# Optimization experiments

Hardware: AMD Instinct MI355X
Metric: run time of the kernel (lower is better)

Reference implementation:

```python
import jax, jax.numpy as jnp
import numpy as np

B, S, H, E, I, TOP_K = 2, 1024, 1024, 8, 1408, 2
W_SCALE = 0.02


def setup_inputs() -> dict:
    key = jax.random.key(0)
    ks = jax.random.split(key, 5)
    return {
        "hidden_states": jax.random.normal(ks[0], (B, S, H), dtype=jnp.float32),
        "router_weight": jax.random.normal(ks[1], (H, E), dtype=jnp.float32) * W_SCALE,
        "gate_proj": jax.random.normal(ks[2], (E, H, I), dtype=jnp.float32) * W_SCALE,
        "up_proj": jax.random.normal(ks[3], (E, H, I), dtype=jnp.float32) * W_SCALE,
        "down_proj": jax.random.normal(ks[4], (E, I, H), dtype=jnp.float32) * W_SCALE,
        "gate_bias": jnp.zeros((E, I), dtype=jnp.float32),
        "up_bias": jnp.zeros((E, I), dtype=jnp.float32),
        "down_bias": jnp.zeros((E, H), dtype=jnp.float32),
        "top_k": TOP_K,
    }


def reference(hidden_states, router_weight, gate_proj, up_proj, down_proj,
              gate_bias, up_bias, down_bias, top_k):
    b, s, h = hidden_states.shape
    e = gate_proj.shape[0]
    x = hidden_states.reshape(-1, h)              # [T, H], T = b*s
    t = x.shape[0]

    # --- RouterAdapter: MoEGate top-k then scatter into dense scores [T, E] ---
    logits = x @ router_weight                    # [T, E]
    probs = jax.nn.softmax(logits, axis=-1)
    topk_w, topk_idx = jax.lax.top_k(probs, top_k)  # [T, k]
    topk_w = topk_w / jnp.sum(topk_w, axis=-1, keepdims=True)  # norm_topk_prob
    scores = jnp.zeros((t, e), dtype=topk_w.dtype)
    scores = scores.at[jnp.arange(t)[:, None], topk_idx].set(topk_w)

    # --- StackedExperts.sparse_forward (dense equivalent of sparse matmuls) ---
    g = jnp.einsum('th,ehi->tei', x, gate_proj) + gate_bias[None]  # [T, E, I]
    u = jnp.einsum('th,ehi->tei', x, up_proj) + up_bias[None]      # [T, E, I]
    act = jax.nn.silu(g) * u                       # ACTIVATION_DEEPSEEK
    d = jnp.einsum('tei,eih->teh', act, down_proj) + down_bias[None]  # [T, E, H]

    # combine per-expert outputs with router scores (non-routed scores are 0,
    # matching the sparse matmul's zero blocks)
    y = jnp.einsum('teh,te->th', d, scores)
    return y.reshape(b, s, h)
```

## Files before the change

### kernel.cpp

```cpp
#include <hip/hip_runtime.h>

#define T_TOK 2048
#define HDIM  1024
#define NEXP  8
#define IDIM  1408

#define BM 128
#define BN 64
#define BK 32
#define KPAD 40
#define MT_SLOTS 16
#define GU_NT 22
#define DN_NT 16
#define DK_HALF 704

typedef __attribute__((ext_vector_type(8))) short bf16x8;
typedef __attribute__((ext_vector_type(4))) float f32x4;

static __device__ __forceinline__ unsigned short f2bf(float f) {
    union { float f; unsigned u; } a; a.f = f;
    return (unsigned short)((a.u + 0x7fffu + ((a.u >> 16) & 1u)) >> 16);
}

__global__ __launch_bounds__(256) void router_compute_kernel(
    const float* __restrict__ x,
    const float* __restrict__ rw,
    int*   __restrict__ sel,
    float* __restrict__ w1arr,
    unsigned short* __restrict__ xb)
{
    __shared__ float rwT[NEXP][HDIM];
    const int tid = threadIdx.x;
#pragma unroll
    for (int p = 0; p < 4; ++p) {
        const int h = tid + 256 * p;
        const float4 a = *(const float4*)(rw + (size_t)h * 8);
        const float4 b = *(const float4*)(rw + (size_t)h * 8 + 4);
        rwT[0][h] = a.x; rwT[1][h] = a.y; rwT[2][h] = a.z; rwT[3][h] = a.w;
        rwT[4][h] = b.x; rwT[5][h] = b.y; rwT[6][h] = b.z; rwT[7][h] = b.w;
    }
    __syncthreads();

    const int wave = (blockIdx.x * blockDim.x + threadIdx.x) >> 6;
    const int lane = threadIdx.x & 63;
    if (wave >= T_TOK) return;
    const int t = wave;

    float xr[16];
    const float* xp = x + (size_t)t * HDIM;
#pragma unroll
    for (int i = 0; i < 16; ++i) xr[i] = xp[lane + 64 * i];

    unsigned short* xbp = xb + (size_t)t * HDIM;
#pragma unroll
    for (int i = 0; i < 16; ++i) xbp[lane + 64 * i] = f2bf(xr[i]);

    double logits[NEXP];
#pragma unroll
    for (int e = 0; e < NEXP; ++e) {
        double s = 0.0;
#pragma unroll
        for (int i = 0; i < 16; ++i)
            s += (double)xr[i] * (double)rwT[e][lane + 64 * i];
#pragma unroll
        for (int off = 32; off > 0; off >>= 1)
            s += __shfl_down(s, off, 64);
        logits[e] = s;
    }

    if (lane == 0) {
        int e1 = 0;
        for (int e = 1; e < NEXP; ++e) if (logits[e] > logits[e1]) e1 = e;
        int e2 = -1;
        for (int e = 0; e < NEXP; ++e) {
            if (e == e1) continue;
            if (e2 < 0 || logits[e] > logits[e2]) e2 = e;
        }
        const double w1 = 1.0 / (1.0 + exp(logits[e2] - logits[e1]));
        sel[t]   = e1 | (e2 << 8);
        w1arr[t] = (float)w1;
    }
}

__global__ __launch_bounds__(1024) void router_scatter_kernel(
    const int* __restrict__ sel, const float* __restrict__ w1arr,
    int* __restrict__ counts,
    int* __restrict__ tok_list, float* __restrict__ wgt_list,
    int* __restrict__ row_list)
{
    __shared__ int cnt[NEXP];
    const int tid = threadIdx.x;
    if (tid < NEXP) cnt[tid] = 0;
    __syncthreads();
    for (int t = tid; t < T_TOK; t += 1024) {
        const int s  = sel[t];
        const int e1 = s & 255, e2 = s >> 8;
        const float w1 = w1arr[t];
        const int p1 = atomicAdd(&cnt[e1], 1);
        tok_list[e1 * T_TOK + p1] = t;
        wgt_list[e1 * T_TOK + p1] = w1;
        row_list[e1 * T_TOK + p1] = 2 * t;
        const int p2 = atomicAdd(&cnt[e2], 1);
        tok_list[e2 * T_TOK + p2] = t;
        wgt_list[e2 * T_TOK + p2] = 1.0f - w1;
        row_list[e2 * T_TOK + p2] = 2 * t + 1;
    }
    __syncthreads();
    if (tid < NEXP) counts[tid] = cnt[tid];
}

__global__ __launch_bounds__(256) void wtrans_all_kernel(
    const float* __restrict__ gw, const float* __restrict__ uw,
    const float* __restrict__ dw,
    unsigned short* __restrict__ gwt, unsigned short* __restrict__ uwt,
    unsigned short* __restrict__ dwt)
{
    const int z  = blockIdx.z;
    const int bx = blockIdx.x;
    const float* src; unsigned short* dst; int K, N, kb, nb;
    if (z < 16) {
        K = HDIM; N = IDIM;
        const int e = z & 7;
        src = (z < 8 ? gw : uw) + (size_t)e * K * N;
        dst = (z < 8 ? gwt : uwt) + (size_t)e * (size_t)N * K;
        nb = bx % 11; kb = bx / 11;
    } else {
        K = IDIM; N = HDIM;
        const int e = z - 16;
        src = dw + (size_t)e * K * N;
        dst = dwt + (size_t)e * (size_t)N * K;
        nb = bx & 7; kb = bx >> 3;
    }

    const int tid  = threadIdx.x;
    const int wv   = tid >> 6;
    const int lane = tid & 63;
    const int k0 = kb * 64 + (wv >> 1) * 32 + (lane >> 4) * 8;
    const int n0 = nb * 128 + (wv & 1) * 64 + (lane & 15) * 4;

    float4 v[8];
#pragma unroll
    for (int r = 0; r < 8; ++r)
        v[r] = *(const float4*)(src + (size_t)(k0 + r) * N + n0);

#pragma unroll
    for (int i = 0; i < 4; ++i) {
        ushort4 lo, hi;
        lo.x = f2bf(((const float*)&v[0])[i]);
        lo.y = f2bf(((const float*)&v[1])[i]);
        lo.z = f2bf(((const float*)&v[2])[i]);
        lo.w = f2bf(((const float*)&v[3])[i]);
        hi.x = f2bf(((const float*)&v[4])[i]);
        hi.y = f2bf(((const float*)&v[5])[i]);
        hi.z = f2bf(((const float*)&v[6])[i]);
        hi.w = f2bf(((const float*)&v[7])[i]);
        unsigned short* dp = dst + (size_t)(n0 + i) * K + k0;
        *(ushort4*)(dp)     = lo;
        *(ushort4*)(dp + 4) = hi;
    }
}

__global__ __launch_bounds__(256) void gateup_kernel(
    const unsigned short* __restrict__ xb,
    const unsigned short* __restrict__ gwt,
    const unsigned short* __restrict__ uwt,
    const float* __restrict__ gb, const float* __restrict__ ub,
    const int* __restrict__ counts,
    const int* __restrict__ tok_list,
    const int* __restrict__ row_list,
    unsigned short* __restrict__ act)
{
    const int flat = blockIdx.x;
    const int xcd  = flat & 7;
    const int q    = flat >> 3;
    const int mt   = q & 15;
    const int slot = q >> 4;
    const int P    = slot * 8 + xcd;
    const int e    = P / GU_NT;
    const int nt   = P % GU_NT;
    const int n_e  = counts[e];
    const int m0   = mt * BM;
    if (m0 >= n_e) return;
    const int n0 = nt * BN;

    const unsigned short* gwp = gwt + (size_t)e * IDIM * HDIM;
    const unsigned short* uwp = uwt + (size_t)e * IDIM * HDIM;
    const float* gbp = gb + (size_t)e * IDIM;
    const float* ubp = ub + (size_t)e * IDIM;

    __shared__ unsigned short As[BM][KPAD];
    __shared__ unsigned short Bg[BN][KPAD];
    __shared__ unsigned short Bu[BN][KPAD];
    __shared__ int gr_lds[BM];
    __shared__ int or_lds[BM];

    const int tid = threadIdx.x;
    const int base = e * T_TOK;
    if (tid < BM) {
        const int m = m0 + tid;
        int g = -1, o = -1;
        if (m < n_e) { g = tok_list[base + m]; o = row_list[base + m]; }
        gr_lds[tid] = g; or_lds[tid] = o;
    }
    __syncthreads();

    const int ar = tid >> 1;
    const int ac = (tid & 1) * 16;
    const int arow = gr_lds[ar];
    const unsigned short* ap = xb + (size_t)(arow < 0 ? 0 : arow) * HDIM;
    const int u   = tid & 127;
    const int brow = u >> 1;
    const int bch  = (u & 1) * 16;
    const unsigned short* bsrc =
        ((tid >> 7) ? uwp : gwp) + (size_t)(n0 + brow) * HDIM + bch;
    unsigned short* Bdst =
        ((tid >> 7) ? &Bu[0][0] : &Bg[0][0]) + brow * KPAD + bch;

    const int wv = tid >> 6, lane = tid & 63;
    const int wm = (wv & 1) * 64, wn = (wv >> 1) * 32;
    const int l16 = lane & 15, quad = lane >> 4;

    f32x4 accg[4][2], accu[4][2];
    const f32x4 zero = {0.0f, 0.0f, 0.0f, 0.0f};
#pragma unroll
    for (int i = 0; i < 4; ++i)
#pragma unroll
        for (int j = 0; j < 2; ++j) { accg[i][j] = zero; accu[i][j] = zero; }

    uint4 PA0 = {0,0,0,0}, PA1 = {0,0,0,0}, PB0, PB1;
    if (arow >= 0) {
        PA0 = *(const uint4*)(ap + ac);
        PA1 = *(const uint4*)(ap + ac + 8);
    }
    PB0 = *(const uint4*)(bsrc);
    PB1 = *(const uint4*)(bsrc + 8);

    for (int k0 = 0; k0 < HDIM; k0 += BK) {
        __syncthreads();
        *(uint4*)&As[ar][ac]       = PA0;
        *(uint4*)&As[ar][ac + 8]   = PA1;
        *(uint4*)(Bdst)            = PB0;
        *(uint4*)(Bdst + 8)        = PB1;
        __syncthreads();

        const int kn = k0 + BK;
        if (kn < HDIM) {
            if (arow >= 0) {
                PA0 = *(const uint4*)(ap + kn + ac);
                PA1 = *(const uint4*)(ap + kn + ac + 8);
            }
            PB0 = *(const uint4*)(bsrc + kn);
            PB1 = *(const uint4*)(bsrc + kn + 8);
        }

        bf16x8 af[4], bgf[2], buf[2];
#pragma unroll
        for (int i = 0; i < 4; ++i)
            af[i] = *(const bf16x8*)&As[wm + i * 16 + l16][quad * 8];
#pragma unroll
        for (int j = 0; j < 2; ++j) {
            bgf[j] = *(const bf16x8*)&Bg[wn + j * 16 + l16][quad * 8];
            buf[j] = *(const bf16x8*)&Bu[wn + j * 16 + l16][quad * 8];
        }
#pragma unroll
        for (int i = 0; i < 4; ++i)
#pragma unroll
            for (int j = 0; j < 2; ++j) {
                accg[i][j] = __builtin_amdgcn_mfma_f32_16x16x32_bf16(
                    af[i], bgf[j], accg[i][j], 0, 0, 0);
                accu[i][j] = __builtin_amdgcn_mfma_f32_16x16x32_bf16(
                    af[i], buf[j], accu[i][j], 0, 0, 0);
            }
    }

#pragma unroll
    for (int j = 0; j < 2; ++j) {
        const int nl = n0 + wn + j * 16 + l16;
        const float gbv = gbp[nl];
        const float ubv = ubp[nl];
#pragma unroll
        for (int i = 0; i < 4; ++i) {
#pragma unroll
            for (int ii = 0; ii < 4; ++ii) {
                const int ml = wm + i * 16 + quad * 4 + ii;
                const int orow = or_lds[ml];
                if (orow >= 0) {
                    const float g = accg[i][j][ii] + gbv;
                    const float uu = accu[i][j][ii] + ubv;
                    act[(size_t)orow * IDIM + nl] =
                        f2bf(g * uu / (1.0f + __expf(-g)));
                }
            }
        }
    }
}

__global__ __launch_bounds__(256) void down_kernel(
    const unsigned short* __restrict__ act,
    const unsigned short* __restrict__ dwt,
    const float* __restrict__ db,
    const int* __restrict__ counts,
    const float* __restrict__ wgt_list,
    const int* __restrict__ row_list,
    float* __restrict__ y2)
{
    const int flat = blockIdx.x;
    const int xcd  = flat & 7;
    const int q    = flat >> 3;
    const int mt   = q & 15;
    const int slot = q >> 4;
    const int P    = slot * 8 + xcd;
    const int sk   = P & 1;
    const int en   = P >> 1;
    const int e    = en >> 4;
    const int nt   = en & 15;
    const int n_e  = counts[e];
    const int m0   = mt * BM;
    if (m0 >= n_e) return;
    const int n0 = nt * BN;
    const int ks = sk * DK_HALF;
    float* y2s = y2 + (size_t)sk * 2 * T_TOK * HDIM;

    const unsigned short* dwp = dwt + (size_t)e * HDIM * IDIM;
    const float* dbp = db + (size_t)e * HDIM;

    __shared__ unsigned short As[BM][KPAD];
    __shared__ unsigned short Bs[BN][KPAD];
    __shared__ int   r_lds[BM];
    __shared__ float w_lds[BM];

    const int tid = threadIdx.x;
    const int base = e * T_TOK;
    if (tid < BM) {
        const int m = m0 + tid;
        int r = -1; float w = 0.0f;
        if (m < n_e) { r = row_list[base + m]; w = wgt_list[base + m]; }
        r_lds[tid] = r; w_lds[tid] = w;
    }
    __syncthreads();

    const int ar = tid >> 1;
    const int ac = (tid & 1) * 16;
    const int arow = r_lds[ar];
    const unsigned short* ap = act + (size_t)(arow < 0 ? 0 : arow) * IDIM + ks;
    const int brow = tid >> 2;
    const int bch  = (tid & 3) * 8;
    const unsigned short* bsrc = dwp + (size_t)(n0 + brow) * IDIM + ks + bch;
    unsigned short* Bdst = &Bs[0][0] + brow * KPAD + bch;

    const int wv = tid >> 6, lane = tid & 63;
    const int wm = (wv & 1) * 64, wn = (wv >> 1) * 32;
    const int l16 = lane & 15, quad = lane >> 4;

    f32x4 acc[4][2];
    const f32x4 zero = {0.0f, 0.0f, 0.0f, 0.0f};
#pragma unroll
    for (int i = 0; i < 4; ++i)
#pragma unroll
        for (int j = 0; j < 2; ++j) acc[i][j] = zero;

    uint4 PA0 = {0,0,0,0}, PA1 = {0,0,0,0}, PB;
    if (arow >= 0) {
        PA0 = *(const uint4*)(ap + ac);
        PA1 = *(const uint4*)(ap + ac + 8);
    }
    PB = *(const uint4*)(bsrc);

    for (int k0 = 0; k0 < DK_HALF; k0 += BK) {
        __syncthreads();
        *(uint4*)&As[ar][ac]     = PA0;
        *(uint4*)&As[ar][ac + 8] = PA1;
        *(uint4*)(Bdst)          = PB;
        __syncthreads();

        const int kn = k0 + BK;
        if (kn < DK_HALF) {
            if (arow >= 0) {
                PA0 = *(const uint4*)(ap + kn + ac);
                PA1 = *(const uint4*)(ap + kn + ac + 8);
            }
            PB = *(const uint4*)(bsrc + kn);
        }

        bf16x8 af[4], bfr[2];
#pragma unroll
        for (int i = 0; i < 4; ++i)
            af[i] = *(const bf16x8*)&As[wm + i * 16 + l16][quad * 8];
#pragma unroll
        for (int j = 0; j < 2; ++j)
            bfr[j] = *(const bf16x8*)&Bs[wn + j * 16 + l16][quad * 8];
#pragma unroll
        for (int i = 0; i < 4; ++i)
#pragma unroll
            for (int j = 0; j < 2; ++j)
                acc[i][j] = __builtin_amdgcn_mfma_f32_16x16x32_bf16(
                    af[i], bfr[j], acc[i][j], 0, 0, 0);
    }

#pragma unroll
    for (int j = 0; j < 2; ++j) {
        const int nl = n0 + wn + j * 16 + l16;
        const float bv = (sk == 0) ? dbp[nl] : 0.0f;
#pragma unroll
        for (int i = 0; i < 4; ++i) {
#pragma unroll
            for (int ii = 0; ii < 4; ++ii) {
                const int ml = wm + i * 16 + quad * 4 + ii;
                const int rr = r_lds[ml];
                if (rr >= 0)
                    y2s[(size_t)rr * HDIM + nl] = w_lds[ml] * (acc[i][j][ii] + bv);
            }
        }
    }
}

__global__ __launch_bounds__(256) void combine_kernel(
    const float* __restrict__ y2, float* __restrict__ out)
{
    const int idx = (blockIdx.x * 256 + threadIdx.x) * 4;
    const int t = idx >> 10;
    const int h = idx & 1023;
    const float* y2b = y2 + (size_t)2 * T_TOK * HDIM;
    const float4 a0 = *(const float4*)(y2  + ((size_t)2 * t) * HDIM + h);
    const float4 a1 = *(const float4*)(y2  + ((size_t)2 * t + 1) * HDIM + h);
    const float4 b0 = *(const float4*)(y2b + ((size_t)2 * t) * HDIM + h);
    const float4 b1 = *(const float4*)(y2b + ((size_t)2 * t + 1) * HDIM + h);
    float4 o;
    o.x = a0.x + a1.x + b0.x + b1.x;
    o.y = a0.y + a1.y + b0.y + b1.y;
    o.z = a0.z + a1.z + b0.z + b1.z;
    o.w = a0.w + a1.w + b0.w + b1.w;
    *(float4*)(out + idx) = o;
}

extern "C" void kernel_launch(void* const* d_in, const int* in_sizes, int n_in,
                              void* d_out, int out_size, void* d_ws, size_t ws_size,
                              hipStream_t stream)
{
    const float* x      = (const float*)d_in[0];
    const float* rw     = (const float*)d_in[1];
    const float* gate_w = (const float*)d_in[2];
    const float* up_w   = (const float*)d_in[3];
    const float* down_w = (const float*)d_in[4];
    const float* gate_b = (const float*)d_in[5];
    const float* up_b   = (const float*)d_in[6];
    const float* down_b = (const float*)d_in[7];
    float* out = (float*)d_out;

    char* ws = (char*)d_ws;
    size_t off = 0;
    int*   counts   = (int*)(ws + off);  off += 256;
    int*   tok_list = (int*)(ws + off);  off += 65536;
    float* wgt_list = (float*)(ws + off); off += 65536;
    int*   row_list = (int*)(ws + off);  off += 65536;
    int*   sel      = (int*)(ws + off);  off += T_TOK * 4;
    float* w1arr    = (float*)(ws + off); off += T_TOK * 4;
    unsigned short* x_bf = (unsigned short*)(ws + off); off += (size_t)T_TOK * HDIM * 2;
    unsigned short* act  = (unsigned short*)(ws + off); off += (size_t)2 * T_TOK * IDIM * 2;
    unsigned short* dwt  = (unsigned short*)(ws + off); off += (size_t)NEXP * IDIM * HDIM * 2;
    unsigned short* gwt  = (unsigned short*)(ws + off); off += (size_t)NEXP * IDIM * HDIM * 2;
    unsigned short* uwt  = (unsigned short*)(ws + off);
    float* y2 = (float*)gwt;

    wtrans_all_kernel<<<dim3(176, 1, 24), 256, 0, stream>>>(
        gate_w, up_w, down_w, gwt, uwt, dwt);

    router_compute_kernel<<<T_TOK / 4, 256, 0, stream>>>(x, rw, sel, w1arr, x_bf);

    router_scatter_kernel<<<1, 1024, 0, stream>>>(
        sel, w1arr, counts, tok_list, wgt_list, row_list);

    gateup_kernel<<<8 * GU_NT * MT_SLOTS, 256, 0, stream>>>(
        x_bf, gwt, uwt, gate_b, up_b, counts, tok_list, row_list, act);

    down_kernel<<<2 * 8 * DN_NT * MT_SLOTS, 256, 0, stream>>>(
        act, dwt, down_b, counts, wgt_list, row_list, y2);

    combine_kernel<<<(T_TOK * HDIM / 4) / 256, 256, 0, stream>>>(y2, out);
}
```

Before: 288.4 us.

## Stage weight transpose through LDS and use 8-wave GEMM blocks

The fp32-to-bf16 weight transpose kernel now writes into an LDS tile and then emits coalesced 16-byte row writes, instead of scattered 8-byte stores. The gate/up and down GEMM kernels move to 512 threads, so each of 8 waves computes a 32x32 sub-tile and each thread issues one 16-byte load per tile. The intent is better latency hiding and write coalescing, at the cost of less MFMA work per wave and more LDS fragment reads.

```diff
diff --git a/kernel.cpp b/kernel.cpp
--- a/kernel.cpp
+++ b/kernel.cpp
@@ -131,36 +131,38 @@
         dst = dwt + (size_t)e * (size_t)N * K;
         nb = bx & 7; kb = bx >> 3;
     }
-
-    const int tid  = threadIdx.x;
-    const int wv   = tid >> 6;
-    const int lane = tid & 63;
-    const int k0 = kb * 64 + (wv >> 1) * 32 + (lane >> 4) * 8;
-    const int n0 = nb * 128 + (wv & 1) * 64 + (lane & 15) * 4;
-
-    float4 v[8];
-#pragma unroll
-    for (int r = 0; r < 8; ++r)
-        v[r] = *(const float4*)(src + (size_t)(k0 + r) * N + n0);
-
-#pragma unroll
-    for (int i = 0; i < 4; ++i) {
-        ushort4 lo, hi;
-        lo.x = f2bf(((const float*)&v[0])[i]);
-        lo.y = f2bf(((const float*)&v[1])[i]);
-        lo.z = f2bf(((const float*)&v[2])[i]);
-        lo.w = f2bf(((const float*)&v[3])[i]);
-        hi.x = f2bf(((const float*)&v[4])[i]);
-        hi.y = f2bf(((const float*)&v[5])[i]);
-        hi.z = f2bf(((const float*)&v[6])[i]);
-        hi.w = f2bf(((const float*)&v[7])[i]);
-        unsigned short* dp = dst + (size_t)(n0 + i) * K + k0;
-        *(ushort4*)(dp)     = lo;
-        *(ushort4*)(dp + 4) = hi;
-    }
-}
-
-__global__ __launch_bounds__(256) void gateup_kernel(
+    const int k0 = kb * 64;
+    const int n0 = nb * 128;
+
+    __shared__ unsigned short tb[128][66];
+
+    const int tid = threadIdx.x;
+    const int lk = tid >> 5;
+    const int ln = (tid & 31) * 4;
+#pragma unroll
+    for (int r = 0; r < 8; ++r) {
+        const int k = r * 8 + lk;
+        const float4 v = *(const float4*)(src + (size_t)(k0 + k) * N + n0 + ln);
+        tb[ln + 0][k] = f2bf(v.x);
+        tb[ln + 1][k] = f2bf(v.y);
+        tb[ln + 2][k] = f2bf(v.z);
+        tb[ln + 3][k] = f2bf(v.w);
+    }
+    __syncthreads();
+
+    const int wn = tid >> 3;
+    const int wk = (tid & 7) * 8;
+#pragma unroll
+    for (int p = 0; p < 4; ++p) {
+        const int n = p * 32 + wn;
+        const unsigned* rp = (const unsigned*)&tb[n][wk];
+        uint4 o;
+        o.x = rp[0]; o.y = rp[1]; o.z = rp[2]; o.w = rp[3];
+        *(uint4*)(dst + (size_t)(n0 + n) * K + k0 + wk) = o;
+    }
+}
+
+__global__ __launch_bounds__(512, 4) void gateup_kernel(
     const unsigned short* __restrict__ xb,
     const unsigned short* __restrict__ gwt,
     const unsigned short* __restrict__ uwt,
@@ -204,72 +206,63 @@
     }
     __syncthreads();
 
-    const int ar = tid >> 1;
-    const int ac = (tid & 1) * 16;
+    const int ar = tid >> 2;
+    const int ac = (tid & 3) * 8;
     const int arow = gr_lds[ar];
-    const unsigned short* ap = xb + (size_t)(arow < 0 ? 0 : arow) * HDIM;
-    const int u   = tid & 127;
-    const int brow = u >> 1;
-    const int bch  = (u & 1) * 16;
+    const unsigned short* ap = xb + (size_t)(arow < 0 ? 0 : arow) * HDIM + ac;
+    unsigned short* Adst = &As[0][0] + ar * KPAD + ac;
+    const int u    = tid & 255;
+    const int brow = u >> 2;
+    const int bch  = (u & 3) * 8;
     const unsigned short* bsrc =
-        ((tid >> 7) ? uwp : gwp) + (size_t)(n0 + brow) * HDIM + bch;
+        ((tid >> 8) ? uwp : gwp) + (size_t)(n0 + brow) * HDIM + bch;
     unsigned short* Bdst =
-        ((tid >> 7) ? &Bu[0][0] : &Bg[0][0]) + brow * KPAD + bch;
+        ((tid >> 8) ? &Bu[0][0] : &Bg[0][0]) + brow * KPAD + bch;
 
     const int wv = tid >> 6, lane = tid & 63;
-    const int wm = (wv & 1) * 64, wn = (wv >> 1) * 32;
+    const int wm = (wv & 3) * 32, wn = (wv >> 2) * 32;
     const int l16 = lane & 15, quad = lane >> 4;
 
-    f32x4 accg[4][2], accu[4][2];
+    f32x4 accg[2][2], accu[2][2];
     const f32x4 zero = {0.0f, 0.0f, 0.0f, 0.0f};
 #pragma unroll
-    for (int i = 0; i < 4; ++i)
+    for (int i = 0; i < 2; ++i)
 #pragma unroll
         for (int j = 0; j < 2; ++j) { accg[i][j] = zero; accu[i][j] = zero; }
 
-    uint4 PA0 = {0,0,0,0}, PA1 = {0,0,0,0}, PB0, PB1;
-    if (arow >= 0) {
-        PA0 = *(const uint4*)(ap + ac);
-        PA1 = *(const uint4*)(ap + ac + 8);
-    }
-    PB0 = *(const uint4*)(bsrc);
-    PB1 = *(const uint4*)(bsrc + 8);
+    uint4 PA = {0, 0, 0, 0}, PB;
+    if (arow >= 0) PA = *(const uint4*)(ap);
+    PB = *(const uint4*)(bsrc);
 
     for (int k0 = 0; k0 < HDIM; k0 += BK) {
         __syncthreads();
-        *(uint4*)&As[ar][ac]       = PA0;
-        *(uint4*)&As[ar][ac + 8]   = PA1;
-        *(uint4*)(Bdst)            = PB0;
-        *(uint4*)(Bdst + 8)        = PB1;
+        *(uint4*)Adst = PA;
+        *(uint4*)Bdst = PB;
         __syncthreads();
 
         const int kn = k0 + BK;
         if (kn < HDIM) {
-            if (arow >= 0) {
-                PA0 = *(const uint4*)(ap + kn + ac);
-                PA1 = *(const uint4*)(ap + kn + ac + 8);
-            }
-            PB0 = *(const uint4*)(bsrc + kn);
-            PB1 = *(const uint4*)(bsrc + kn + 8);
-        }
-
-        bf16x8 af[4], bgf[2], buf[2];
-#pragma unroll
-        for (int i = 0; i < 4; ++i)
+            if (arow >= 0) PA = *(const uint4*)(ap + kn);
+            PB = *(const uint4*)(bsrc + kn);
+        }
+
+        bf16x8 af[2], bgf[2], buf_[2];
+#pragma unroll
+        for (int i = 0; i < 2; ++i)
             af[i] = *(const bf16x8*)&As[wm + i * 16 + l16][quad * 8];
 #pragma unroll
         for (int j = 0; j < 2; ++j) {
-            bgf[j] = *(const bf16x8*)&Bg[wn + j * 16 + l16][quad * 8];
-            buf[j] = *(const bf16x8*)&Bu[wn + j * 16 + l16][quad * 8];
-        }
-#pragma unroll
-        for (int i = 0; i < 4; ++i)
+            bgf[j]  = *(const bf16x8*)&Bg[wn + j * 16 + l16][quad * 8];
+            buf_[j] = *(const bf16x8*)&Bu[wn + j * 16 + l16][quad * 8];
+        }
+#pragma unroll
+        for (int i = 0; i < 2; ++i)
 #pragma unroll
             for (int j = 0; j < 2; ++j) {
                 accg[i][j] = __builtin_amdgcn_mfma_f32_16x16x32_bf16(
                     af[i], bgf[j], accg[i][j], 0, 0, 0);
                 accu[i][j] = __builtin_amdgcn_mfma_f32_16x16x32_bf16(
-                    af[i], buf[j], accu[i][j], 0, 0, 0);
+                    af[i], buf_[j], accu[i][j], 0, 0, 0);
             }
     }
 
@@ -279,7 +272,7 @@
         const float gbv = gbp[nl];
         const float ubv = ubp[nl];
 #pragma unroll
-        for (int i = 0; i < 4; ++i) {
+        for (int i = 0; i < 2; ++i) {
 #pragma unroll
             for (int ii = 0; ii < 4; ++ii) {
                 const int ml = wm + i * 16 + quad * 4 + ii;
@@ -295,7 +288,7 @@
     }
 }
 
-__global__ __launch_bounds__(256) void down_kernel(
+__global__ __launch_bounds__(512, 4) void down_kernel(
     const unsigned short* __restrict__ act,
     const unsigned short* __restrict__ dwt,
     const float* __restrict__ db,
@@ -339,58 +332,54 @@
     }
     __syncthreads();
 
-    const int ar = tid >> 1;
-    const int ac = (tid & 1) * 16;
+    const int ar = tid >> 2;
+    const int ac = (tid & 3) * 8;
     const int arow = r_lds[ar];
-    const unsigned short* ap = act + (size_t)(arow < 0 ? 0 : arow) * IDIM + ks;
-    const int brow = tid >> 2;
+    const unsigned short* ap =
+        act + (size_t)(arow < 0 ? 0 : arow) * IDIM + ks + ac;
+    unsigned short* Adst = &As[0][0] + ar * KPAD + ac;
+    const bool hasB = tid < 256;
+    const int brow = (tid & 255) >> 2;
     const int bch  = (tid & 3) * 8;
     const unsigned short* bsrc = dwp + (size_t)(n0 + brow) * IDIM + ks + bch;
     unsigned short* Bdst = &Bs[0][0] + brow * KPAD + bch;
 
     const int wv = tid >> 6, lane = tid & 63;
-    const int wm = (wv & 1) * 64, wn = (wv >> 1) * 32;
+    const int wm = (wv & 3) * 32, wn = (wv >> 2) * 32;
     const int l16 = lane & 15, quad = lane >> 4;
 
-    f32x4 acc[4][2];
+    f32x4 acc[2][2];
     const f32x4 zero = {0.0f, 0.0f, 0.0f, 0.0f};
 #pragma unroll
-    for (int i = 0; i < 4; ++i)
+    for (int i = 0; i < 2; ++i)
 #pragma unroll
         for (int j = 0; j < 2; ++j) acc[i][j] = zero;
 
-    uint4 PA0 = {0,0,0,0}, PA1 = {0,0,0,0}, PB;
-    if (arow >= 0) {
-        PA0 = *(const uint4*)(ap + ac);
-        PA1 = *(const uint4*)(ap + ac + 8);
-    }
-    PB = *(const uint4*)(bsrc);
+    uint4 PA = {0, 0, 0, 0}, PB = {0, 0, 0, 0};
+    if (arow >= 0) PA = *(const uint4*)(ap);
+    if (hasB) PB = *(const uint4*)(bsrc);
 
     for (int k0 = 0; k0 < DK_HALF; k0 += BK) {
         __syncthreads();
-        *(uint4*)&As[ar][ac]     = PA0;
-        *(uint4*)&As[ar][ac + 8] = PA1;
-        *(uint4*)(Bdst)          = PB;
+        *(uint4*)Adst = PA;
+        if (hasB) *(uint4*)Bdst = PB;
         __syncthreads();
 
         const int kn = k0 + BK;
         if (kn < DK_HALF) {
-            if (arow >= 0) {
-                PA0 = *(const uint4*)(ap + kn + ac);
-                PA1 = *(const uint4*)(ap + kn + ac + 8);
-            }
-            PB = *(const uint4*)(bsrc + kn);
-        }
-
-        bf16x8 af[4], bfr[2];
-#pragma unroll
-        for (int i = 0; i < 4; ++i)
+            if (arow >= 0) PA = *(const uint4*)(ap + kn);
+            if (hasB) PB = *(const uint4*)(bsrc + kn);
+        }
+
+        bf16x8 af[2], bfr[2];
+#pragma unroll
+        for (int i = 0; i < 2; ++i)
             af[i] = *(const bf16x8*)&As[wm + i * 16 + l16][quad * 8];
 #pragma unroll
         for (int j = 0; j < 2; ++j)
             bfr[j] = *(const bf16x8*)&Bs[wn + j * 16 + l16][quad * 8];
 #pragma unroll
-        for (int i = 0; i < 4; ++i)
+        for (int i = 0; i < 2; ++i)
 #pragma unroll
             for (int j = 0; j < 2; ++j)
                 acc[i][j] = __builtin_amdgcn_mfma_f32_16x16x32_bf16(
@@ -402,7 +391,7 @@
         const int nl = n0 + wn + j * 16 + l16;
         const float bv = (sk == 0) ? dbp[nl] : 0.0f;
 #pragma unroll
-        for (int i = 0; i < 4; ++i) {
+        for (int i = 0; i < 2; ++i) {
 #pragma unroll
             for (int ii = 0; ii < 4; ++ii) {
                 const int ml = wm + i * 16 + quad * 4 + ii;
@@ -470,10 +459,10 @@
     router_scatter_kernel<<<1, 1024, 0, stream>>>(
         sel, w1arr, counts, tok_list, wgt_list, row_list);
 
-    gateup_kernel<<<8 * GU_NT * MT_SLOTS, 256, 0, stream>>>(
+    gateup_kernel<<<8 * GU_NT * MT_SLOTS, 512, 0, stream>>>(
         x_bf, gwt, uwt, gate_b, up_b, counts, tok_list, row_list, act);
 
-    down_kernel<<<2 * 8 * DN_NT * MT_SLOTS, 256, 0, stream>>>(
+    down_kernel<<<2 * 8 * DN_NT * MT_SLOTS, 512, 0, stream>>>(
         act, dwt, down_b, counts, wgt_list, row_list, y2);
 
     combine_kernel<<<(T_TOK * HDIM / 4) / 256, 256, 0, stream>>>(y2, out);
```

Result: slower. 295.9 us (+2.6%).

## Double GEMM K-tile to 64 and stage weight transpose through LDS

Applied to the files above, without the earlier changes.

The gate/up and down GEMM kernels now use a 64-wide K tile (padded LDS rows of 72), so each main-loop iteration loads twice as much data and issues two MFMA sub-steps per pair of barriers. This halves the number of synchronisations and loop iterations. The cost is more prefetch registers and more LDS per block. Separately, the weight transpose/convert kernel now stages through a shared-memory tile so its global stores are coalesced 16-byte row writes instead of scattered 8-byte writes. DK_HALF=704 is divisible by 64, so the down kernel's K loop stays exact.

```diff
diff --git a/kernel.cpp b/kernel.cpp
--- a/kernel.cpp
+++ b/kernel.cpp
@@ -7,8 +7,8 @@
 
 #define BM 128
 #define BN 64
-#define BK 32
-#define KPAD 40
+#define BK 64
+#define KPAD 72
 #define MT_SLOTS 16
 #define GU_NT 22
 #define DN_NT 16
@@ -131,32 +131,34 @@
         dst = dwt + (size_t)e * (size_t)N * K;
         nb = bx & 7; kb = bx >> 3;
     }
-
-    const int tid  = threadIdx.x;
-    const int wv   = tid >> 6;
-    const int lane = tid & 63;
-    const int k0 = kb * 64 + (wv >> 1) * 32 + (lane >> 4) * 8;
-    const int n0 = nb * 128 + (wv & 1) * 64 + (lane & 15) * 4;
-
-    float4 v[8];
-#pragma unroll
-    for (int r = 0; r < 8; ++r)
-        v[r] = *(const float4*)(src + (size_t)(k0 + r) * N + n0);
-
-#pragma unroll
-    for (int i = 0; i < 4; ++i) {
-        ushort4 lo, hi;
-        lo.x = f2bf(((const float*)&v[0])[i]);
-        lo.y = f2bf(((const float*)&v[1])[i]);
-        lo.z = f2bf(((const float*)&v[2])[i]);
-        lo.w = f2bf(((const float*)&v[3])[i]);
-        hi.x = f2bf(((const float*)&v[4])[i]);
-        hi.y = f2bf(((const float*)&v[5])[i]);
-        hi.z = f2bf(((const float*)&v[6])[i]);
-        hi.w = f2bf(((const float*)&v[7])[i]);
-        unsigned short* dp = dst + (size_t)(n0 + i) * K + k0;
-        *(ushort4*)(dp)     = lo;
-        *(ushort4*)(dp + 4) = hi;
+    const int k0 = kb * 64;
+    const int n0 = nb * 128;
+
+    __shared__ unsigned short tb[128][66];
+
+    const int tid = threadIdx.x;
+    const int lk = tid >> 5;
+    const int ln = (tid & 31) * 4;
+#pragma unroll
+    for (int r = 0; r < 8; ++r) {
+        const int k = r * 8 + lk;
+        const float4 v = *(const float4*)(src + (size_t)(k0 + k) * N + n0 + ln);
+        tb[ln + 0][k] = f2bf(v.x);
+        tb[ln + 1][k] = f2bf(v.y);
+        tb[ln + 2][k] = f2bf(v.z);
+        tb[ln + 3][k] = f2bf(v.w);
+    }
+    __syncthreads();
+
+    const int wn = tid >> 3;
+    const int wk = (tid & 7) * 8;
+#pragma unroll
+    for (int p = 0; p < 4; ++p) {
+        const int n = p * 32 + wn;
+        const unsigned* rp = (const unsigned*)&tb[n][wk];
+        uint4 o;
+        o.x = rp[0]; o.y = rp[1]; o.z = rp[2]; o.w = rp[3];
+        *(uint4*)(dst + (size_t)(n0 + n) * K + k0 + wk) = o;
     }
 }
 
@@ -205,12 +207,13 @@
     __syncthreads();
 
     const int ar = tid >> 1;
-    const int ac = (tid & 1) * 16;
+    const int ac = (tid & 1) * 32;
     const int arow = gr_lds[ar];
-    const unsigned short* ap = xb + (size_t)(arow < 0 ? 0 : arow) * HDIM;
-    const int u   = tid & 127;
+    const unsigned short* ap = xb + (size_t)(arow < 0 ? 0 : arow) * HDIM + ac;
+    unsigned short* Adst = &As[0][0] + ar * KPAD + ac;
+    const int u    = tid & 127;
     const int brow = u >> 1;
-    const int bch  = (u & 1) * 16;
+    const int bch  = (u & 1) * 32;
     const unsigned short* bsrc =
         ((tid >> 7) ? uwp : gwp) + (size_t)(n0 + brow) * HDIM + bch;
     unsigned short* Bdst =
@@ -227,50 +230,67 @@
 #pragma unroll
         for (int j = 0; j < 2; ++j) { accg[i][j] = zero; accu[i][j] = zero; }
 
-    uint4 PA0 = {0,0,0,0}, PA1 = {0,0,0,0}, PB0, PB1;
+    uint4 PA0 = {0,0,0,0}, PA1 = {0,0,0,0}, PA2 = {0,0,0,0}, PA3 = {0,0,0,0};
+    uint4 PB0, PB1, PB2, PB3;
     if (arow >= 0) {
-        PA0 = *(const uint4*)(ap + ac);
-        PA1 = *(const uint4*)(ap + ac + 8);
+        PA0 = *(const uint4*)(ap);
+        PA1 = *(const uint4*)(ap + 8);
+        PA2 = *(const uint4*)(ap + 16);
+        PA3 = *(const uint4*)(ap + 24);
     }
     PB0 = *(const uint4*)(bsrc);
     PB1 = *(const uint4*)(bsrc + 8);
+    PB2 = *(const uint4*)(bsrc + 16);
+    PB3 = *(const uint4*)(bsrc + 24);
 
     for (int k0 = 0; k0 < HDIM; k0 += BK) {
         __syncthreads();
-        *(uint4*)&As[ar][ac]       = PA0;
-        *(uint4*)&As[ar][ac + 8]   = PA1;
-        *(uint4*)(Bdst)            = PB0;
-        *(uint4*)(Bdst + 8)        = PB1;
+        *(uint4*)(Adst)      = PA0;
+        *(uint4*)(Adst + 8)  = PA1;
+        *(uint4*)(Adst + 16) = PA2;
+        *(uint4*)(Adst + 24) = PA3;
+        *(uint4*)(Bdst)      = PB0;
+        *(uint4*)(Bdst + 8)  = PB1;
+        *(uint4*)(Bdst + 16) = PB2;
+        *(uint4*)(Bdst + 24) = PB3;
         __syncthreads();
 
         const int kn = k0 + BK;
         if (kn < HDIM) {
             if (arow >= 0) {
-                PA0 = *(const uint4*)(ap + kn + ac);
-                PA1 = *(const uint4*)(ap + kn + ac + 8);
+                PA0 = *(const uint4*)(ap + kn);
+                PA1 = *(const uint4*)(ap + kn + 8);
+                PA2 = *(const uint4*)(ap + kn + 16);
+                PA3 = *(const uint4*)(ap + kn + 24);
             }
             PB0 = *(const uint4*)(bsrc + kn);
             PB1 = *(const uint4*)(bsrc + kn + 8);
-        }
-
-        bf16x8 af[4], bgf[2], buf[2];
-#pragma unroll
-        for (int i = 0; i < 4; ++i)
-            af[i] = *(const bf16x8*)&As[wm + i * 16 + l16][quad * 8];
-#pragma unroll
-        for (int j = 0; j < 2; ++j) {
-            bgf[j] = *(const bf16x8*)&Bg[wn + j * 16 + l16][quad * 8];
-            buf[j] = *(const bf16x8*)&Bu[wn + j * 16 + l16][quad * 8];
-        }
-#pragma unroll
-        for (int i = 0; i < 4; ++i)
+            PB2 = *(const uint4*)(bsrc + kn + 16);
+            PB3 = *(const uint4*)(bsrc + kn + 24);
+        }
+
+#pragma unroll
+        for (int ks = 0; ks < 2; ++ks) {
+            const int kc = ks * 32 + quad * 8;
+            bf16x8 af[4], bgf[2], buf_[2];
+#pragma unroll
+            for (int i = 0; i < 4; ++i)
+                af[i] = *(const bf16x8*)&As[wm + i * 16 + l16][kc];
 #pragma unroll
             for (int j = 0; j < 2; ++j) {
-                accg[i][j] = __builtin_amdgcn_mfma_f32_16x16x32_bf16(
-                    af[i], bgf[j], accg[i][j], 0, 0, 0);
-                accu[i][j] = __builtin_amdgcn_mfma_f32_16x16x32_bf16(
-                    af[i], buf[j], accu[i][j], 0, 0, 0);
+                bgf[j]  = *(const bf16x8*)&Bg[wn + j * 16 + l16][kc];
+                buf_[j] = *(const bf16x8*)&Bu[wn + j * 16 + l16][kc];
             }
+#pragma unroll
+            for (int i = 0; i < 4; ++i)
+#pragma unroll
+                for (int j = 0; j < 2; ++j) {
+                    accg[i][j] = __builtin_amdgcn_mfma_f32_16x16x32_bf16(
+                        af[i], bgf[j], accg[i][j], 0, 0, 0);
+                    accu[i][j] = __builtin_amdgcn_mfma_f32_16x16x32_bf16(
+                        af[i], buf_[j], accu[i][j], 0, 0, 0);
+                }
+        }
     }
 
 #pragma unroll
@@ -340,11 +360,13 @@
     __syncthreads();
 
     const int ar = tid >> 1;
-    const int ac = (tid & 1) * 16;
+    const int ac = (tid & 1) * 32;
     const int arow = r_lds[ar];
-    const unsigned short* ap = act + (size_t)(arow < 0 ? 0 : arow) * IDIM + ks;
+    const unsigned short* ap =
+        act + (size_t)(arow < 0 ? 0 : arow) * IDIM + ks + ac;
+    unsigned short* Adst = &As[0][0] + ar * KPAD + ac;
     const int brow = tid >> 2;
-    const int bch  = (tid & 3) * 8;
+    const int bch  = (tid & 3) * 16;
     const unsigned short* bsrc = dwp + (size_t)(n0 + brow) * IDIM + ks + bch;
     unsigned short* Bdst = &Bs[0][0] + brow * KPAD + bch;
 
@@ -359,42 +381,56 @@
 #pragma unroll
         for (int j = 0; j < 2; ++j) acc[i][j] = zero;
 
-    uint4 PA0 = {0,0,0,0}, PA1 = {0,0,0,0}, PB;
+    uint4 PA0 = {0,0,0,0}, PA1 = {0,0,0,0}, PA2 = {0,0,0,0}, PA3 = {0,0,0,0};
+    uint4 PB0, PB1;
     if (arow >= 0) {
-        PA0 = *(const uint4*)(ap + ac);
-        PA1 = *(const uint4*)(ap + ac + 8);
-    }
-    PB = *(const uint4*)(bsrc);
+        PA0 = *(const uint4*)(ap);
+        PA1 = *(const uint4*)(ap + 8);
+        PA2 = *(const uint4*)(ap + 16);
+        PA3 = *(const uint4*)(ap + 24);
+    }
+    PB0 = *(const uint4*)(bsrc);
+    PB1 = *(const uint4*)(bsrc + 8);
 
     for (int k0 = 0; k0 < DK_HALF; k0 += BK) {
         __syncthreads();
-        *(uint4*)&As[ar][ac]     = PA0;
-        *(uint4*)&As[ar][ac + 8] = PA1;
-        *(uint4*)(Bdst)          = PB;
+        *(uint4*)(Adst)      = PA0;
+        *(uint4*)(Adst + 8)  = PA1;
+        *(uint4*)(Adst + 16) = PA2;
+        *(uint4*)(Adst + 24) = PA3;
+        *(uint4*)(Bdst)      = PB0;
+        *(uint4*)(Bdst + 8)  = PB1;
         __syncthreads();
 
         const int kn = k0 + BK;
         if (kn < DK_HALF) {
             if (arow >= 0) {
-                PA0 = *(const uint4*)(ap + kn + ac);
-                PA1 = *(const uint4*)(ap + kn + ac + 8);
+                PA0 = *(const uint4*)(ap + kn);
+                PA1 = *(const uint4*)(ap + kn + 8);
+                PA2 = *(const uint4*)(ap + kn + 16);
+                PA3 = *(const uint4*)(ap + kn + 24);
             }
-            PB = *(const uint4*)(bsrc + kn);
-        }
-
-        bf16x8 af[4], bfr[2];
-#pragma unroll
-        for (int i = 0; i < 4; ++i)
-            af[i] = *(const bf16x8*)&As[wm + i * 16 + l16][quad * 8];
-#pragma unroll
-        for (int j = 0; j < 2; ++j)
-            bfr[j] = *(const bf16x8*)&Bs[wn + j * 16 + l16][quad * 8];
-#pragma unroll
-        for (int i = 0; i < 4; ++i)
+            PB0 = *(const uint4*)(bsrc + kn);
+            PB1 = *(const uint4*)(bsrc + kn + 8);
+        }
+
+#pragma unroll
+        for (int ks2 = 0; ks2 < 2; ++ks2) {
+            const int kc = ks2 * 32 + quad * 8;
+            bf16x8 af[4], bfr[2];
+#pragma unroll
+            for (int i = 0; i < 4; ++i)
+                af[i] = *(const bf16x8*)&As[wm + i * 16 + l16][kc];
 #pragma unroll
             for (int j = 0; j < 2; ++j)
-                acc[i][j] = __builtin_amdgcn_mfma_f32_16x16x32_bf16(
-                    af[i], bfr[j], acc[i][j], 0, 0, 0);
+                bfr[j] = *(const bf16x8*)&Bs[wn + j * 16 + l16][kc];
+#pragma unroll
+            for (int i = 0; i < 4; ++i)
+#pragma unroll
+                for (int j = 0; j < 2; ++j)
+                    acc[i][j] = __builtin_amdgcn_mfma_f32_16x16x32_bf16(
+                        af[i], bfr[j], acc[i][j], 0, 0, 0);
+        }
     }
 
 #pragma unroll
```

After: 294.9 us. 2.2% more time.

## Fuse weight fp32-to-bf16 conversion and transpose into GEMM tile loads

Applied to the files above, without the earlier changes.

Removes the separate weight transpose/convert pre-pass. The gate/up and down GEMM kernels now read fp32 weights directly in their native [K,N] layout, convert them to bf16 in registers and write them transposed into shared memory. This avoids writing and re-reading about 70 MB of bf16 weights plus one kernel launch. In exchange, every M-tile block re-reads and re-converts the fp32 weights, which doubles per-block weight bytes and adds conversion ALU work and scattered LDS stores inside the main loop.

```diff
diff --git a/kernel.cpp b/kernel.cpp
--- a/kernel.cpp
+++ b/kernel.cpp
@@ -109,61 +109,10 @@
     if (tid < NEXP) counts[tid] = cnt[tid];
 }
 
-__global__ __launch_bounds__(256) void wtrans_all_kernel(
-    const float* __restrict__ gw, const float* __restrict__ uw,
-    const float* __restrict__ dw,
-    unsigned short* __restrict__ gwt, unsigned short* __restrict__ uwt,
-    unsigned short* __restrict__ dwt)
-{
-    const int z  = blockIdx.z;
-    const int bx = blockIdx.x;
-    const float* src; unsigned short* dst; int K, N, kb, nb;
-    if (z < 16) {
-        K = HDIM; N = IDIM;
-        const int e = z & 7;
-        src = (z < 8 ? gw : uw) + (size_t)e * K * N;
-        dst = (z < 8 ? gwt : uwt) + (size_t)e * (size_t)N * K;
-        nb = bx % 11; kb = bx / 11;
-    } else {
-        K = IDIM; N = HDIM;
-        const int e = z - 16;
-        src = dw + (size_t)e * K * N;
-        dst = dwt + (size_t)e * (size_t)N * K;
-        nb = bx & 7; kb = bx >> 3;
-    }
-
-    const int tid  = threadIdx.x;
-    const int wv   = tid >> 6;
-    const int lane = tid & 63;
-    const int k0 = kb * 64 + (wv >> 1) * 32 + (lane >> 4) * 8;
-    const int n0 = nb * 128 + (wv & 1) * 64 + (lane & 15) * 4;
-
-    float4 v[8];
-#pragma unroll
-    for (int r = 0; r < 8; ++r)
-        v[r] = *(const float4*)(src + (size_t)(k0 + r) * N + n0);
-
-#pragma unroll
-    for (int i = 0; i < 4; ++i) {
-        ushort4 lo, hi;
-        lo.x = f2bf(((const float*)&v[0])[i]);
-        lo.y = f2bf(((const float*)&v[1])[i]);
-        lo.z = f2bf(((const float*)&v[2])[i]);
-        lo.w = f2bf(((const float*)&v[3])[i]);
-        hi.x = f2bf(((const float*)&v[4])[i]);
-        hi.y = f2bf(((const float*)&v[5])[i]);
-        hi.z = f2bf(((const float*)&v[6])[i]);
-        hi.w = f2bf(((const float*)&v[7])[i]);
-        unsigned short* dp = dst + (size_t)(n0 + i) * K + k0;
-        *(ushort4*)(dp)     = lo;
-        *(ushort4*)(dp + 4) = hi;
-    }
-}
-
 __global__ __launch_bounds__(256) void gateup_kernel(
     const unsigned short* __restrict__ xb,
-    const unsigned short* __restrict__ gwt,
-    const unsigned short* __restrict__ uwt,
+    const float* __restrict__ gw,
+    const float* __restrict__ uw,
     const float* __restrict__ gb, const float* __restrict__ ub,
     const int* __restrict__ counts,
     const int* __restrict__ tok_list,
@@ -183,8 +132,8 @@
     if (m0 >= n_e) return;
     const int n0 = nt * BN;
 
-    const unsigned short* gwp = gwt + (size_t)e * IDIM * HDIM;
-    const unsigned short* uwp = uwt + (size_t)e * IDIM * HDIM;
+    const float* gwp = gw + (size_t)e * HDIM * IDIM;
+    const float* uwp = uw + (size_t)e * HDIM * IDIM;
     const float* gbp = gb + (size_t)e * IDIM;
     const float* ubp = ub + (size_t)e * IDIM;
 
@@ -208,13 +157,12 @@
     const int ac = (tid & 1) * 16;
     const int arow = gr_lds[ar];
     const unsigned short* ap = xb + (size_t)(arow < 0 ? 0 : arow) * HDIM;
-    const int u   = tid & 127;
-    const int brow = u >> 1;
-    const int bch  = (u & 1) * 16;
-    const unsigned short* bsrc =
-        ((tid >> 7) ? uwp : gwp) + (size_t)(n0 + brow) * HDIM + bch;
-    unsigned short* Bdst =
-        ((tid >> 7) ? &Bu[0][0] : &Bg[0][0]) + brow * KPAD + bch;
+    const int u  = tid & 127;
+    const int kq = (u >> 4) * 4;
+    const int nc = (u & 15) * 4;
+    const float* bp =
+        ((tid >> 7) ? uwp : gwp) + (size_t)kq * IDIM + n0 + nc;
+    unsigned short* Bb = ((tid >> 7) ? &Bu[0][0] : &Bg[0][0]);
 
     const int wv = tid >> 6, lane = tid & 63;
     const int wm = (wv & 1) * 64, wn = (wv >> 1) * 32;
@@ -227,20 +175,30 @@
 #pragma unroll
         for (int j = 0; j < 2; ++j) { accg[i][j] = zero; accu[i][j] = zero; }
 
-    uint4 PA0 = {0,0,0,0}, PA1 = {0,0,0,0}, PB0, PB1;
+    uint4 PA0 = {0,0,0,0}, PA1 = {0,0,0,0};
+    float4 PB0, PB1, PB2, PB3;
     if (arow >= 0) {
         PA0 = *(const uint4*)(ap + ac);
         PA1 = *(const uint4*)(ap + ac + 8);
     }
-    PB0 = *(const uint4*)(bsrc);
-    PB1 = *(const uint4*)(bsrc + 8);
+    PB0 = *(const float4*)(bp);
+    PB1 = *(const float4*)(bp + IDIM);
+    PB2 = *(const float4*)(bp + 2 * IDIM);
+    PB3 = *(const float4*)(bp + 3 * IDIM);
 
     for (int k0 = 0; k0 < HDIM; k0 += BK) {
         __syncthreads();
-        *(uint4*)&As[ar][ac]       = PA0;
-        *(uint4*)&As[ar][ac + 8]   = PA1;
-        *(uint4*)(Bdst)            = PB0;
-        *(uint4*)(Bdst + 8)        = PB1;
+        *(uint4*)&As[ar][ac]     = PA0;
+        *(uint4*)&As[ar][ac + 8] = PA1;
+#pragma unroll
+        for (int i = 0; i < 4; ++i) {
+            ushort4 w;
+            w.x = f2bf(((const float*)&PB0)[i]);
+            w.y = f2bf(((const float*)&PB1)[i]);
+            w.z = f2bf(((const float*)&PB2)[i]);
+            w.w = f2bf(((const float*)&PB3)[i]);
+            *(ushort4*)(Bb + (size_t)(nc + i) * KPAD + kq) = w;
+        }
         __syncthreads();
 
         const int kn = k0 + BK;
@@ -249,18 +207,21 @@
                 PA0 = *(const uint4*)(ap + kn + ac);
                 PA1 = *(const uint4*)(ap + kn + ac + 8);
             }
-            PB0 = *(const uint4*)(bsrc + kn);
-            PB1 = *(const uint4*)(bsrc + kn + 8);
-        }
-
-        bf16x8 af[4], bgf[2], buf[2];
+            const float* bq = bp + (size_t)kn * IDIM;
+            PB0 = *(const float4*)(bq);
+            PB1 = *(const float4*)(bq + IDIM);
+            PB2 = *(const float4*)(bq + 2 * IDIM);
+            PB3 = *(const float4*)(bq + 3 * IDIM);
+        }
+
+        bf16x8 af[4], bgf[2], buf_[2];
 #pragma unroll
         for (int i = 0; i < 4; ++i)
             af[i] = *(const bf16x8*)&As[wm + i * 16 + l16][quad * 8];
 #pragma unroll
         for (int j = 0; j < 2; ++j) {
-            bgf[j] = *(const bf16x8*)&Bg[wn + j * 16 + l16][quad * 8];
-            buf[j] = *(const bf16x8*)&Bu[wn + j * 16 + l16][quad * 8];
+            bgf[j]  = *(const bf16x8*)&Bg[wn + j * 16 + l16][quad * 8];
+            buf_[j] = *(const bf16x8*)&Bu[wn + j * 16 + l16][quad * 8];
         }
 #pragma unroll
         for (int i = 0; i < 4; ++i)
@@ -269,7 +230,7 @@
                 accg[i][j] = __builtin_amdgcn_mfma_f32_16x16x32_bf16(
                     af[i], bgf[j], accg[i][j], 0, 0, 0);
                 accu[i][j] = __builtin_amdgcn_mfma_f32_16x16x32_bf16(
-                    af[i], buf[j], accu[i][j], 0, 0, 0);
+                    af[i], buf_[j], accu[i][j], 0, 0, 0);
             }
     }
 
@@ -297,7 +258,7 @@
 
 __global__ __launch_bounds__(256) void down_kernel(
     const unsigned short* __restrict__ act,
-    const unsigned short* __restrict__ dwt,
+    const float* __restrict__ dw,
     const float* __restrict__ db,
     const int* __restrict__ counts,
     const float* __restrict__ wgt_list,
@@ -321,7 +282,7 @@
     const int ks = sk * DK_HALF;
     float* y2s = y2 + (size_t)sk * 2 * T_TOK * HDIM;
 
-    const unsigned short* dwp = dwt + (size_t)e * HDIM * IDIM;
+    const float* dwp = dw + (size_t)e * IDIM * HDIM;
     const float* dbp = db + (size_t)e * HDIM;
 
     __shared__ unsigned short As[BM][KPAD];
@@ -343,10 +304,10 @@
     const int ac = (tid & 1) * 16;
     const int arow = r_lds[ar];
     const unsigned short* ap = act + (size_t)(arow < 0 ? 0 : arow) * IDIM + ks;
-    const int brow = tid >> 2;
-    const int bch  = (tid & 3) * 8;
-    const unsigned short* bsrc = dwp + (size_t)(n0 + brow) * IDIM + ks + bch;
-    unsigned short* Bdst = &Bs[0][0] + brow * KPAD + bch;
+    const bool hasB = tid < 128;
+    const int kq = ((tid & 127) >> 4) * 4;
+    const int nc = (tid & 15) * 4;
+    const float* bp = dwp + (size_t)(ks + kq) * HDIM + n0 + nc;
 
     const int wv = tid >> 6, lane = tid & 63;
     const int wm = (wv & 1) * 64, wn = (wv >> 1) * 32;
@@ -359,18 +320,34 @@
 #pragma unroll
         for (int j = 0; j < 2; ++j) acc[i][j] = zero;
 
-    uint4 PA0 = {0,0,0,0}, PA1 = {0,0,0,0}, PB;
+    uint4 PA0 = {0,0,0,0}, PA1 = {0,0,0,0};
+    float4 PB0 = {0,0,0,0}, PB1 = {0,0,0,0}, PB2 = {0,0,0,0}, PB3 = {0,0,0,0};
     if (arow >= 0) {
         PA0 = *(const uint4*)(ap + ac);
         PA1 = *(const uint4*)(ap + ac + 8);
     }
-    PB = *(const uint4*)(bsrc);
+    if (hasB) {
+        PB0 = *(const float4*)(bp);
+        PB1 = *(const float4*)(bp + HDIM);
+        PB2 = *(const float4*)(bp + 2 * HDIM);
+        PB3 = *(const float4*)(bp + 3 * HDIM);
+    }
 
     for (int k0 = 0; k0 < DK_HALF; k0 += BK) {
         __syncthreads();
         *(uint4*)&As[ar][ac]     = PA0;
         *(uint4*)&As[ar][ac + 8] = PA1;
-        *(uint4*)(Bdst)          = PB;
+        if (hasB) {
+#pragma unroll
+            for (int i = 0; i < 4; ++i) {
+                ushort4 w;
+                w.x = f2bf(((const float*)&PB0)[i]);
+                w.y = f2bf(((const float*)&PB1)[i]);
+                w.z = f2bf(((const float*)&PB2)[i]);
+                w.w = f2bf(((const float*)&PB3)[i]);
+                *(ushort4*)(&Bs[0][0] + (size_t)(nc + i) * KPAD + kq) = w;
+            }
+        }
         __syncthreads();
 
         const int kn = k0 + BK;
@@ -379,7 +356,13 @@
                 PA0 = *(const uint4*)(ap + kn + ac);
                 PA1 = *(const uint4*)(ap + kn + ac + 8);
             }
-            PB = *(const uint4*)(bsrc + kn);
+            if (hasB) {
+                const float* bq = bp + (size_t)kn * HDIM;
+                PB0 = *(const float4*)(bq);
+                PB1 = *(const float4*)(bq + HDIM);
+                PB2 = *(const float4*)(bq + 2 * HDIM);
+                PB3 = *(const float4*)(bq + 3 * HDIM);
+            }
         }
 
         bf16x8 af[4], bfr[2];
@@ -457,13 +440,7 @@
     float* w1arr    = (float*)(ws + off); off += T_TOK * 4;
     unsigned short* x_bf = (unsigned short*)(ws + off); off += (size_t)T_TOK * HDIM * 2;
     unsigned short* act  = (unsigned short*)(ws + off); off += (size_t)2 * T_TOK * IDIM * 2;
-    unsigned short* dwt  = (unsigned short*)(ws + off); off += (size_t)NEXP * IDIM * HDIM * 2;
-    unsigned short* gwt  = (unsigned short*)(ws + off); off += (size_t)NEXP * IDIM * HDIM * 2;
-    unsigned short* uwt  = (unsigned short*)(ws + off);
-    float* y2 = (float*)gwt;
-
-    wtrans_all_kernel<<<dim3(176, 1, 24), 256, 0, stream>>>(
-        gate_w, up_w, down_w, gwt, uwt, dwt);
+    float* y2 = (float*)(ws + off);
 
     router_compute_kernel<<<T_TOK / 4, 256, 0, stream>>>(x, rw, sel, w1arr, x_bf);
 
@@ -471,10 +448,10 @@
         sel, w1arr, counts, tok_list, wgt_list, row_list);
 
     gateup_kernel<<<8 * GU_NT * MT_SLOTS, 256, 0, stream>>>(
-        x_bf, gwt, uwt, gate_b, up_b, counts, tok_list, row_list, act);
+        x_bf, gate_w, up_w, gate_b, up_b, counts, tok_list, row_list, act);
 
     down_kernel<<<2 * 8 * DN_NT * MT_SLOTS, 256, 0, stream>>>(
-        act, dwt, down_b, counts, wgt_list, row_list, y2);
+        act, down_w, down_b, counts, wgt_list, row_list, y2);
 
     combine_kernel<<<(T_TOK * HDIM / 4) / 256, 256, 0, stream>>>(y2, out);
 }
```

After: 300.1 us. 4.0% more time.
